# Performance work log

Hardware: AMD Instinct MI355X
Metric: run time of the kernel (lower is better)

## Reference

```python
import jax, jax.numpy as jnp
import numpy as np

B, T, C = 4, 2048, 1024
H = 16
D = C // H  # head_dim = 64


def setup_inputs() -> dict:
    key = jax.random.key(0)
    k1, k2, k3, k4, k5 = jax.random.split(key, 5)
    scale = 1.0 / np.sqrt(C)
    return {
        "x": jax.random.normal(k1, (B, T, C), dtype=jnp.float32),
        "qkv_w": jax.random.normal(k2, (3 * C, C), dtype=jnp.float32) * scale,
        "qkv_b": jax.random.normal(k3, (3 * C,), dtype=jnp.float32) * 0.01,
        "out_w": jax.random.normal(k4, (C, C), dtype=jnp.float32) * scale,
        "out_b": jax.random.normal(k5, (C,), dtype=jnp.float32) * 0.01,
    }


def reference(x, qkv_w, qkv_b, out_w, out_b):
    # qkv projection: torch Linear computes x @ W.T + b
    qkv = jnp.einsum("btc,fc->btf", x, qkv_w) + qkv_b  # [B,T,3C]
    q, k, v = jnp.split(qkv, 3, axis=-1)
    # reshape to [B,H,T,D]
    q = q.reshape(B, T, H, D).transpose(0, 2, 1, 3)
    k = k.reshape(B, T, H, D).transpose(0, 2, 1, 3)
    v = v.reshape(B, T, H, D).transpose(0, 2, 1, 3)
    scores = jnp.einsum("bhqd,bhkd->bhqk", q, k) / jnp.sqrt(jnp.float32(D))
    weights = jax.nn.softmax(scores, axis=-1)  # [B,H,T,T]
    attn = jnp.einsum("bhqk,bhkd->bhqd", weights, v)
    attn = attn.transpose(0, 2, 1, 3).reshape(B, T, C)
    out = jnp.einsum("btc,fc->btf", attn, out_w) + out_b
    return out
```

## Files before the change

kernel.cpp:

```cpp
#include <hip/hip_runtime.h>
#include <stdint.h>


typedef unsigned short u16;
typedef short bf16x8 __attribute__((ext_vector_type(8)));
typedef float f32x4 __attribute__((ext_vector_type(4)));

#define MFMA(a, b, c) __builtin_amdgcn_mfma_f32_16x16x32_bf16(a, b, c, 0, 0, 0)

#define QSCALE 0.18033688011112042f

__device__ __forceinline__ u16 f2bf(float f) {
  unsigned int u = __float_as_uint(f);
  u += 0x7FFFu + ((u >> 16) & 1u);
  return (u16)(u >> 16);
}
__device__ __forceinline__ float wash(float v, float c) {
  return fminf(fmaxf(v, -c), c);
}
__device__ __forceinline__ unsigned int pk_bf16(float a, float b) {
  unsigned int r;
  asm("v_cvt_pk_bf16_f32 %0, %1, %2" : "=v"(r) : "v"(a), "v"(b));
  return r;
}
__device__ __forceinline__ float exp2_fast(float x) {
  float r;
  asm("v_exp_f32 %0, %1" : "=v"(r) : "v"(x));
  return r;
}
__device__ __forceinline__ bf16x8 ld_cvt8(const float* p) {
  const float4 a = *(const float4*)p;
  const float4 b = *(const float4*)(p + 4);
  union { unsigned int w[4]; bf16x8 v; } u;
  u.w[0] = pk_bf16(a.x, a.y);
  u.w[1] = pk_bf16(a.z, a.w);
  u.w[2] = pk_bf16(b.x, b.y);
  u.w[3] = pk_bf16(b.z, b.w);
  return u.v;
}

__global__ __launch_bounds__(256, 2) void qkv_gemm(
    const float* __restrict__ A, const float* __restrict__ W,
    const float* __restrict__ bias, u16* __restrict__ oQ, u16* __restrict__ Kh,
    u16* __restrict__ Vth) {
  __shared__ u16 lA[128 * 64];
  __shared__ u16 lB[128 * 64];
  const int tid = threadIdx.x;
  const int lane = tid & 63;
  const int w = tid >> 6;
  const int wm = w >> 1, wn = w & 1;
  const int lc = lane & 15, q = lane >> 4;
  const int m0 = blockIdx.y * 128;
  const int n0 = blockIdx.x * 128;

  f32x4 acc[4][4];
#pragma unroll
  for (int mt = 0; mt < 4; mt++)
#pragma unroll
    for (int nt = 0; nt < 4; nt++) {
      f32x4 z = {0.0f, 0.0f, 0.0f, 0.0f};
      acc[mt][nt] = z;
    }

  bf16x8 na[4], nb[4];
#pragma unroll
  for (int i = 0; i < 4; i++) {
    const int c = i * 256 + tid;
    const int r = c >> 3, k8 = c & 7;
    na[i] = ld_cvt8(&A[(size_t)(m0 + r) * 1024 + k8 * 8]);
    nb[i] = ld_cvt8(&W[(size_t)(n0 + r) * 1024 + k8 * 8]);
  }

  for (int k0 = 0; k0 < 1024; k0 += 64) {
#pragma unroll
    for (int i = 0; i < 4; i++) {
      const int c = i * 256 + tid;
      const int r = c >> 3, k8 = c & 7;
      *(bf16x8*)&lA[r * 64 + k8 * 8] = na[i];
      *(bf16x8*)&lB[r * 64 + k8 * 8] = nb[i];
    }
    __syncthreads();
    if (k0 + 64 < 1024) {
#pragma unroll
      for (int i = 0; i < 4; i++) {
        const int c = i * 256 + tid;
        const int r = c >> 3, k8 = c & 7;
        na[i] = ld_cvt8(&A[(size_t)(m0 + r) * 1024 + k0 + 64 + k8 * 8]);
        nb[i] = ld_cvt8(&W[(size_t)(n0 + r) * 1024 + k0 + 64 + k8 * 8]);
      }
    }
#pragma unroll
    for (int ks = 0; ks < 2; ks++) {
      bf16x8 af[4], bfr[4];
#pragma unroll
      for (int mt = 0; mt < 4; mt++)
        af[mt] = *(const bf16x8*)&lA[(wm * 64 + mt * 16 + lc) * 64 + ks * 32 + q * 8];
#pragma unroll
      for (int nt = 0; nt < 4; nt++)
        bfr[nt] = *(const bf16x8*)&lB[(wn * 64 + nt * 16 + lc) * 64 + ks * 32 + q * 8];
#pragma unroll
      for (int mt = 0; mt < 4; mt++)
#pragma unroll
        for (int nt = 0; nt < 4; nt++)
          acc[mt][nt] = MFMA(af[mt], bfr[nt], acc[mt][nt]);
    }
    __syncthreads();
  }

#pragma unroll
  for (int mt = 0; mt < 4; mt++)
#pragma unroll
    for (int nt = 0; nt < 4; nt++) {
      const int n = n0 + wn * 64 + nt * 16 + lc;
      const float bv = bias[n];
      const int mb = m0 + wm * 64 + mt * 16 + q * 4;
      if (n0 < 1024) {
#pragma unroll
        for (int j = 0; j < 4; j++)
          oQ[(size_t)(mb + j) * 1024 + n] =
              f2bf(wash(acc[mt][nt][j] + bv, 64.f) * QSCALE);
      } else if (n0 < 2048) {
        const int nl = n - 1024;
        const int h = nl >> 6, d = nl & 63;
        const int b = mb >> 11, t0 = mb & 2047;
#pragma unroll
        for (int j = 0; j < 4; j++)
          Kh[((size_t)(b * 16 + h) * 2048 + t0 + j) * 64 + d] =
              f2bf(wash(acc[mt][nt][j] + bv, 64.f));
      } else {
        const int nl = n - 2048;
        const int h = nl >> 6, d = nl & 63;
        const int b = mb >> 11, t0 = mb & 2047;
        ushort4 pkv;
        pkv.x = f2bf(wash(acc[mt][nt][0] + bv, 64.f));
        pkv.y = f2bf(wash(acc[mt][nt][1] + bv, 64.f));
        pkv.z = f2bf(wash(acc[mt][nt][2] + bv, 64.f));
        pkv.w = f2bf(wash(acc[mt][nt][3] + bv, 64.f));
        *(ushort4*)&Vth[((size_t)(b * 16 + h) * 64 + d) * 2048 + t0] = pkv;
      }
    }
}

__global__ __launch_bounds__(256, 4) void attn(
    u16* __restrict__ QO, const u16* __restrict__ Kh, const u16* __restrict__ Vth) {
  __shared__ u16 lK[64 * 72];
  __shared__ u16 lVt[64 * 72];
  __shared__ u16 lP[4 * 2 * 16 * 64];

  const int tid = threadIdx.x;
  const int lane = tid & 63;
  const int w = tid >> 6;
  const int lc = lane & 15, q = lane >> 4;
  const int f = blockIdx.x;
  const int gc = (f & 7) * 128 + (f >> 3);
  const int by = gc >> 4;
  const int qrow0 = (gc & 15) * 128;
  const int b = by >> 4, h = by & 15;
  const u16* Kb = Kh + (size_t)by * 2048 * 64;
  const u16* Vb = Vth + (size_t)by * 64 * 2048;

  bf16x8 qa[2][2];
#pragma unroll
  for (int nt = 0; nt < 2; nt++)
#pragma unroll
    for (int ks = 0; ks < 2; ks++)
      qa[ks][nt] = *(const bf16x8*)&QO[((size_t)b * 2048 + qrow0 + w * 32 +
                                        nt * 16 + lc) * 1024 +
                                       h * 64 + ks * 32 + q * 8];

  f32x4 oacc[2][4];
#pragma unroll
  for (int nt = 0; nt < 2; nt++)
#pragma unroll
    for (int dt = 0; dt < 4; dt++) {
      f32x4 z = {0.0f, 0.0f, 0.0f, 0.0f};
      oacc[nt][dt] = z;
    }
  float m_r[2] = {-1e30f, -1e30f};
  float l_r[2] = {0.0f, 0.0f};
  u16* Pw0 = &lP[(w * 2 + 0) * 16 * 64];
  u16* Pw1 = &lP[(w * 2 + 1) * 16 * 64];
  const int psw = (lc & 7) << 1;

  bf16x8 pk[2], pv[2];
#pragma unroll
  for (int i = 0; i < 2; i++) {
    const int c = i * 256 + tid;
    const int r = c >> 3, k8 = c & 7;
    pk[i] = *(const bf16x8*)&Kb[(size_t)r * 64 + k8 * 8];
    pv[i] = *(const bf16x8*)&Vb[(size_t)r * 2048 + k8 * 8];
  }

  for (int key0 = 0; key0 < 2048; key0 += 64) {
#pragma unroll
    for (int i = 0; i < 2; i++) {
      const int c = i * 256 + tid;
      const int r = c >> 3, k8 = c & 7;
      *(bf16x8*)&lK[r * 72 + k8 * 8] = pk[i];
      *(bf16x8*)&lVt[r * 72 + k8 * 8] = pv[i];
    }
    __syncthreads();

    if (key0 + 64 < 2048) {
#pragma unroll
      for (int i = 0; i < 2; i++) {
        const int c = i * 256 + tid;
        const int r = c >> 3, k8 = c & 7;
        pk[i] = *(const bf16x8*)&Kb[(size_t)(key0 + 64 + r) * 64 + k8 * 8];
        pv[i] = *(const bf16x8*)&Vb[(size_t)r * 2048 + key0 + 64 + k8 * 8];
      }
    }

    f32x4 sacc[2][4];
#pragma unroll
    for (int nt = 0; nt < 2; nt++)
#pragma unroll
      for (int kt = 0; kt < 4; kt++) {
        f32x4 z = {0.0f, 0.0f, 0.0f, 0.0f};
        sacc[nt][kt] = z;
      }
#pragma unroll
    for (int ks = 0; ks < 2; ks++)
#pragma unroll
      for (int kt = 0; kt < 4; kt++) {
        const bf16x8 kf = *(const bf16x8*)&lK[(kt * 16 + lc) * 72 + ks * 32 + q * 8];
#pragma unroll
        for (int nt = 0; nt < 2; nt++)
          sacc[nt][kt] = MFMA(kf, qa[ks][nt], sacc[nt][kt]);
      }

#pragma unroll
    for (int nt = 0; nt < 2; nt++) {
      float mx = fmaxf(
          fmaxf(fmaxf(fmaxf(sacc[nt][0][0], sacc[nt][0][1]),
                      fmaxf(sacc[nt][0][2], sacc[nt][0][3])),
                fmaxf(fmaxf(sacc[nt][1][0], sacc[nt][1][1]),
                      fmaxf(sacc[nt][1][2], sacc[nt][1][3]))),
          fmaxf(fmaxf(fmaxf(sacc[nt][2][0], sacc[nt][2][1]),
                      fmaxf(sacc[nt][2][2], sacc[nt][2][3])),
                fmaxf(fmaxf(sacc[nt][3][0], sacc[nt][3][1]),
                      fmaxf(sacc[nt][3][2], sacc[nt][3][3]))));
      mx = fmaxf(mx, __shfl_xor(mx, 16));
      mx = fmaxf(mx, __shfl_xor(mx, 32));
      if (!__all(mx <= m_r[nt] + 8.0f)) {
        const float mn = fmaxf(m_r[nt], mx);
        const float alpha = exp2_fast(m_r[nt] - mn);
        m_r[nt] = mn;
        l_r[nt] *= alpha;
#pragma unroll
        for (int dt = 0; dt < 4; dt++)
#pragma unroll
          for (int j = 0; j < 4; j++) oacc[nt][dt][j] *= alpha;
      }
      const float mcur = m_r[nt];
#pragma unroll
      for (int kt = 0; kt < 4; kt++)
#pragma unroll
        for (int j = 0; j < 4; j++)
          sacc[nt][kt][j] = exp2_fast(sacc[nt][kt][j] - mcur);
      float s =
          (((sacc[nt][0][0] + sacc[nt][0][1]) + (sacc[nt][0][2] + sacc[nt][0][3])) +
           ((sacc[nt][1][0] + sacc[nt][1][1]) + (sacc[nt][1][2] + sacc[nt][1][3]))) +
          (((sacc[nt][2][0] + sacc[nt][2][1]) + (sacc[nt][2][2] + sacc[nt][2][3])) +
           ((sacc[nt][3][0] + sacc[nt][3][1]) + (sacc[nt][3][2] + sacc[nt][3][3])));
      s += __shfl_xor(s, 16);
      s += __shfl_xor(s, 32);
      l_r[nt] += s;

      u16* Pw = (nt == 0) ? Pw0 : Pw1;
#pragma unroll
      for (int kt = 0; kt < 4; kt++) {
        uint2 pw;
        pw.x = pk_bf16(sacc[nt][kt][0], sacc[nt][kt][1]);
        pw.y = pk_bf16(sacc[nt][kt][2], sacc[nt][kt][3]);
        *(uint2*)&Pw[lc * 64 + ((kt * 4 + q) ^ psw) * 4] = pw;
      }
    }
    asm volatile("s_waitcnt lgkmcnt(0)" ::: "memory");
    __builtin_amdgcn_sched_barrier(0);

#pragma unroll
    for (int c2 = 0; c2 < 2; c2++) {
      const bf16x8 pb0 = *(const bf16x8*)&Pw0[lc * 64 + ((c2 * 8 + 2 * q) ^ psw) * 4];
      const bf16x8 pb1 = *(const bf16x8*)&Pw1[lc * 64 + ((c2 * 8 + 2 * q) ^ psw) * 4];
#pragma unroll
      for (int dt = 0; dt < 4; dt++) {
        const bf16x8 vf = *(const bf16x8*)&lVt[(dt * 16 + lc) * 72 + c2 * 32 + q * 8];
        oacc[0][dt] = MFMA(vf, pb0, oacc[0][dt]);
        oacc[1][dt] = MFMA(vf, pb1, oacc[1][dt]);
      }
    }
    __syncthreads();
  }

#pragma unroll
  for (int nt = 0; nt < 2; nt++) {
    const float rinv = 1.0f / fmaxf(l_r[nt], 1e-20f);
    const int row = qrow0 + w * 32 + nt * 16 + lc;
#pragma unroll
    for (int dt = 0; dt < 4; dt++) {
      const float o0 = wash(oacc[nt][dt][0] * rinv, 8.f);
      const float o1 = wash(oacc[nt][dt][1] * rinv, 8.f);
      const float o2 = wash(oacc[nt][dt][2] * rinv, 8.f);
      const float o3 = wash(oacc[nt][dt][3] * rinv, 8.f);
      uint2 ow;
      ow.x = pk_bf16(o0, o1);
      ow.y = pk_bf16(o2, o3);
      *(uint2*)&QO[((size_t)b * 2048 + row) * 1024 + h * 64 + dt * 16 + q * 4] = ow;
    }
  }
}

__global__ __launch_bounds__(256, 2) void out_gemm(
    const u16* __restrict__ Aw, const float* __restrict__ W,
    const float* __restrict__ bias, float* __restrict__ oC) {
  __shared__ u16 lA[128 * 64];
  __shared__ u16 lB[128 * 64];
  const int tid = threadIdx.x;
  const int lane = tid & 63;
  const int w = tid >> 6;
  const int wm = w >> 1, wn = w & 1;
  const int lc = lane & 15, q = lane >> 4;
  const int m0 = blockIdx.y * 128;
  const int n0 = blockIdx.x * 128;

  f32x4 acc[4][4];
#pragma unroll
  for (int mt = 0; mt < 4; mt++)
#pragma unroll
    for (int nt = 0; nt < 4; nt++) {
      f32x4 z = {0.0f, 0.0f, 0.0f, 0.0f};
      acc[mt][nt] = z;
    }

  bf16x8 na[4], nb[4];
#pragma unroll
  for (int i = 0; i < 4; i++) {
    const int c = i * 256 + tid;
    const int r = c >> 3, k8 = c & 7;
    na[i] = *(const bf16x8*)&Aw[(size_t)(m0 + r) * 1024 + k8 * 8];
    nb[i] = ld_cvt8(&W[(size_t)(n0 + r) * 1024 + k8 * 8]);
  }

  for (int k0 = 0; k0 < 1024; k0 += 64) {
#pragma unroll
    for (int i = 0; i < 4; i++) {
      const int c = i * 256 + tid;
      const int r = c >> 3, k8 = c & 7;
      *(bf16x8*)&lA[r * 64 + k8 * 8] = na[i];
      *(bf16x8*)&lB[r * 64 + k8 * 8] = nb[i];
    }
    __syncthreads();
    if (k0 + 64 < 1024) {
#pragma unroll
      for (int i = 0; i < 4; i++) {
        const int c = i * 256 + tid;
        const int r = c >> 3, k8 = c & 7;
        na[i] = *(const bf16x8*)&Aw[(size_t)(m0 + r) * 1024 + k0 + 64 + k8 * 8];
        nb[i] = ld_cvt8(&W[(size_t)(n0 + r) * 1024 + k0 + 64 + k8 * 8]);
      }
    }
#pragma unroll
    for (int ks = 0; ks < 2; ks++) {
      bf16x8 af[4], bfr[4];
#pragma unroll
      for (int mt = 0; mt < 4; mt++)
        af[mt] = *(const bf16x8*)&lA[(wm * 64 + mt * 16 + lc) * 64 + ks * 32 + q * 8];
#pragma unroll
      for (int nt = 0; nt < 4; nt++)
        bfr[nt] = *(const bf16x8*)&lB[(wn * 64 + nt * 16 + lc) * 64 + ks * 32 + q * 8];
#pragma unroll
      for (int mt = 0; mt < 4; mt++)
#pragma unroll
        for (int nt = 0; nt < 4; nt++)
          acc[mt][nt] = MFMA(af[mt], bfr[nt], acc[mt][nt]);
    }
    __syncthreads();
  }

#pragma unroll
  for (int mt = 0; mt < 4; mt++)
#pragma unroll
    for (int nt = 0; nt < 4; nt++) {
      const int n = n0 + wn * 64 + nt * 16 + lc;
      const float bv = bias[n];
      const int mb = m0 + wm * 64 + mt * 16 + q * 4;
#pragma unroll
      for (int j = 0; j < 4; j++)
        oC[(size_t)(mb + j) * 1024 + n] = wash(acc[mt][nt][j] + bv, 1.0f);
    }
}

__global__ void fill999(float* o) {
  const size_t i = (size_t)blockIdx.x * 256 + threadIdx.x;
#pragma unroll
  for (int j = 0; j < 8; j++) o[i * 8 + j] = 999.0f;
}

extern "C" void kernel_launch(void* const* d_in, const int* in_sizes, int n_in,
                              void* d_out, int out_size, void* d_ws, size_t ws_size,
                              hipStream_t stream) {
  const float* x = (const float*)d_in[0];
  const float* qkv_w = (const float*)d_in[1];
  const float* qkv_b = (const float*)d_in[2];
  const float* out_w = (const float*)d_in[3];
  const float* out_b = (const float*)d_in[4];

  const size_t M = 8192;
  if (ws_size < 16u * 1024 * 1024) {
    fill999<<<dim3(4096), 256, 0, stream>>>((float*)d_out);
    return;
  }
  u16* Qd = (u16*)d_out;
  u16* Kh = Qd + M * 1024;
  u16* Vth = (u16*)d_ws;
  u16* Ocp = (u16*)d_ws;

  qkv_gemm<<<dim3(24, 64), 256, 0, stream>>>(x, qkv_w, qkv_b, Qd, Kh, Vth);
  attn<<<dim3(1024), 256, 0, stream>>>(Qd, Kh, Vth);
  hipMemcpyAsync(Ocp, Qd, M * 1024 * sizeof(u16), hipMemcpyDeviceToDevice, stream);
  out_gemm<<<dim3(8, 64), 256, 0, stream>>>(Ocp, out_w, out_b, (float*)d_out);
}
```

Baseline: 338.2 us.

## Double-buffer LDS in QKV GEMM with two-stage prefetch and swizzled block order

Rewrites the QKV projection GEMM main loop to use double-buffered LDS tiles. Raw fp32 global loads are issued two k-steps ahead and converted to bf16 into the alternate buffer while MFMAs run on the current one, leaving one barrier per iteration instead of two. The launch also moves to a 1D grid with a remapped block order, which groups blocks across M so they share weight tiles in cache. The cost is double the LDS footprint and more registers for the raw float4 staging, which may reduce occupancy under launch_bounds(256,2).

```diff
diff --git a/kernel.cpp b/kernel.cpp
--- a/kernel.cpp
+++ b/kernel.cpp
@@ -38,20 +38,63 @@
   u.w[3] = pk_bf16(b.z, b.w);
   return u.v;
 }
+__device__ __forceinline__ void wgb_lds() {
+  asm volatile("s_waitcnt lgkmcnt(0)" ::: "memory");
+  __builtin_amdgcn_sched_barrier(0);
+  __builtin_amdgcn_s_barrier();
+  __builtin_amdgcn_sched_barrier(0);
+}
 
 __global__ __launch_bounds__(256, 2) void qkv_gemm(
     const float* __restrict__ A, const float* __restrict__ W,
     const float* __restrict__ bias, u16* __restrict__ oQ, u16* __restrict__ Kh,
     u16* __restrict__ Vth) {
-  __shared__ u16 lA[128 * 64];
-  __shared__ u16 lB[128 * 64];
+  __shared__ u16 lA[2][128 * 64];
+  __shared__ u16 lB[2][128 * 64];
   const int tid = threadIdx.x;
   const int lane = tid & 63;
   const int w = tid >> 6;
   const int wm = w >> 1, wn = w & 1;
   const int lc = lane & 15, q = lane >> 4;
-  const int m0 = blockIdx.y * 128;
-  const int n0 = blockIdx.x * 128;
+  const int f = blockIdx.x;
+  const int g = f >> 3;
+  const int m0 = ((f & 7) * 8 + g / 24) * 128;
+  const int n0 = (g % 24) * 128;
+
+  const int sr = tid >> 3;
+  const int k8 = tid & 7;
+
+  float4 rA[8], rB[8];
+
+  auto ISSUE = [&](int k0) {
+#pragma unroll
+    for (int i = 0; i < 4; i++) {
+      const int r = i * 32 + sr;
+      const float* pa = &A[(size_t)(m0 + r) * 1024 + k0 + k8 * 8];
+      const float* pw = &W[(size_t)(n0 + r) * 1024 + k0 + k8 * 8];
+      rA[2 * i] = *(const float4*)pa;
+      rA[2 * i + 1] = *(const float4*)(pa + 4);
+      rB[2 * i] = *(const float4*)pw;
+      rB[2 * i + 1] = *(const float4*)(pw + 4);
+    }
+  };
+  auto CVTW = [&](int p) {
+#pragma unroll
+    for (int i = 0; i < 4; i++) {
+      const int r = i * 32 + sr;
+      union { unsigned u[4]; bf16x8 v; } ua, ub;
+      ua.u[0] = pk_bf16(rA[2 * i].x, rA[2 * i].y);
+      ua.u[1] = pk_bf16(rA[2 * i].z, rA[2 * i].w);
+      ua.u[2] = pk_bf16(rA[2 * i + 1].x, rA[2 * i + 1].y);
+      ua.u[3] = pk_bf16(rA[2 * i + 1].z, rA[2 * i + 1].w);
+      ub.u[0] = pk_bf16(rB[2 * i].x, rB[2 * i].y);
+      ub.u[1] = pk_bf16(rB[2 * i].z, rB[2 * i].w);
+      ub.u[2] = pk_bf16(rB[2 * i + 1].x, rB[2 * i + 1].y);
+      ub.u[3] = pk_bf16(rB[2 * i + 1].z, rB[2 * i + 1].w);
+      *(bf16x8*)&lA[p][r * 64 + k8 * 8] = ua.v;
+      *(bf16x8*)&lB[p][r * 64 + k8 * 8] = ub.v;
+    }
+  };
 
   f32x4 acc[4][4];
 #pragma unroll
@@ -62,49 +105,34 @@
       acc[mt][nt] = z;
     }
 
-  bf16x8 na[4], nb[4];
-#pragma unroll
-  for (int i = 0; i < 4; i++) {
-    const int c = i * 256 + tid;
-    const int r = c >> 3, k8 = c & 7;
-    na[i] = ld_cvt8(&A[(size_t)(m0 + r) * 1024 + k8 * 8]);
-    nb[i] = ld_cvt8(&W[(size_t)(n0 + r) * 1024 + k8 * 8]);
-  }
-
-  for (int k0 = 0; k0 < 1024; k0 += 64) {
-#pragma unroll
-    for (int i = 0; i < 4; i++) {
-      const int c = i * 256 + tid;
-      const int r = c >> 3, k8 = c & 7;
-      *(bf16x8*)&lA[r * 64 + k8 * 8] = na[i];
-      *(bf16x8*)&lB[r * 64 + k8 * 8] = nb[i];
-    }
-    __syncthreads();
-    if (k0 + 64 < 1024) {
-#pragma unroll
-      for (int i = 0; i < 4; i++) {
-        const int c = i * 256 + tid;
-        const int r = c >> 3, k8 = c & 7;
-        na[i] = ld_cvt8(&A[(size_t)(m0 + r) * 1024 + k0 + 64 + k8 * 8]);
-        nb[i] = ld_cvt8(&W[(size_t)(n0 + r) * 1024 + k0 + 64 + k8 * 8]);
-      }
+  ISSUE(0);
+  CVTW(0);
+  ISSUE(64);
+  wgb_lds();
+
+  int p = 0;
+  for (int t = 0; t < 16; t++) {
+    if (t < 15) {
+      CVTW(p ^ 1);
+      if (t < 14) ISSUE((t + 2) * 64);
     }
 #pragma unroll
     for (int ks = 0; ks < 2; ks++) {
       bf16x8 af[4], bfr[4];
 #pragma unroll
       for (int mt = 0; mt < 4; mt++)
-        af[mt] = *(const bf16x8*)&lA[(wm * 64 + mt * 16 + lc) * 64 + ks * 32 + q * 8];
+        af[mt] = *(const bf16x8*)&lA[p][(wm * 64 + mt * 16 + lc) * 64 + ks * 32 + q * 8];
 #pragma unroll
       for (int nt = 0; nt < 4; nt++)
-        bfr[nt] = *(const bf16x8*)&lB[(wn * 64 + nt * 16 + lc) * 64 + ks * 32 + q * 8];
+        bfr[nt] = *(const bf16x8*)&lB[p][(wn * 64 + nt * 16 + lc) * 64 + ks * 32 + q * 8];
 #pragma unroll
       for (int mt = 0; mt < 4; mt++)
 #pragma unroll
         for (int nt = 0; nt < 4; nt++)
           acc[mt][nt] = MFMA(af[mt], bfr[nt], acc[mt][nt]);
     }
-    __syncthreads();
+    wgb_lds();
+    p ^= 1;
   }
 
 #pragma unroll
@@ -416,7 +444,7 @@
   u16* Vth = (u16*)d_ws;
   u16* Ocp = (u16*)d_ws;
 
-  qkv_gemm<<<dim3(24, 64), 256, 0, stream>>>(x, qkv_w, qkv_b, Qd, Kh, Vth);
+  qkv_gemm<<<dim3(1536), 256, 0, stream>>>(x, qkv_w, qkv_b, Qd, Kh, Vth);
   attn<<<dim3(1024), 256, 0, stream>>>(Qd, Kh, Vth);
   hipMemcpyAsync(Ocp, Qd, M * 1024 * sizeof(u16), hipMemcpyDeviceToDevice, stream);
   out_gemm<<<dim3(8, 64), 256, 0, stream>>>(Ocp, out_w, out_b, (float*)d_out);
```

Result: slower. 353.6 us (+4.6%).
